# Optimization experiments

Hardware: AMD Instinct MI355X
Metric: run time of the kernel (lower is better)

The kernel has to match this reference:

```python
import jax, jax.numpy as jnp
import numpy as np

NUM_HEADS = 16

def setup_inputs() -> dict:
    key = jax.random.key(0)
    ks = jax.random.split(key, 9)
    B, S, H = 2, 2048, 1024
    sc = 0.02
    return {
        "x":  jax.random.normal(ks[0], (B, S, H), jnp.float32),
        "Wq": jax.random.normal(ks[1], (H, H), jnp.float32) * sc,
        "bq": jnp.zeros((H,), jnp.float32),
        "Wk": jax.random.normal(ks[2], (H, H), jnp.float32) * sc,
        "bk": jnp.zeros((H,), jnp.float32),
        "Wv": jax.random.normal(ks[3], (H, H), jnp.float32) * sc,
        "bv": jnp.zeros((H,), jnp.float32),
        "Wo": jax.random.normal(ks[4], (H, H), jnp.float32) * sc,
        "bo": jnp.zeros((H,), jnp.float32),
    }

def _split_heads(t, nh):
    B, S, H = t.shape
    return t.reshape(B, S, nh, H // nh).transpose(0, 2, 1, 3)  # [B, nh, S, hd]

def reference(x, Wq, bq, Wk, bk, Wv, bv, Wo, bo):
    # mask_type == 'gaussian', dropout = 0 (eval), return_weights = False
    B, S, H = x.shape
    nh = NUM_HEADS
    q = _split_heads(x @ Wq + bq, nh)  # [B, nh, S, hd]
    k = _split_heads(x @ Wk + bk, nh)
    v = _split_heads(x @ Wv + bv, nh)
    dif = q - k  # elementwise, as in the original
    # exp(-dif @ dif^T / 2)
    score = jnp.exp(-0.5 * jnp.einsum('bhqd,bhkd->bhqk', dif, dif))
    # gaussian mask: 1 strictly above the diagonal, 0 on/below (faithful to source)
    mask = jnp.triu(jnp.ones((S, S), x.dtype), k=1)
    prob = score * mask  # [B, nh, S, S]
    ctx = jnp.einsum('bhqk,bhkd->bhqd', prob, v)  # [B, nh, S, hd]
    ctx = ctx.transpose(0, 2, 1, 3).reshape(B, S, H)
    return ctx @ Wo + bo
```

## Files before the change

kernel.cpp:

```cpp
#include <hip/hip_runtime.h>
#include <math.h>

constexpr int SEQ  = 2048;
constexpr int HID  = 1024;
constexpr int MTOT = 4096;
constexpr int BH   = 32;

typedef _Float16 f16;
typedef _Float16 f16x8 __attribute__((ext_vector_type(8)));
typedef float    f32x4 __attribute__((ext_vector_type(4)));

__global__ __launch_bounds__(256) void prep(const float* __restrict__ x,
                                            const float* __restrict__ Wq,
                                            const float* __restrict__ Wk,
                                            const float* __restrict__ Wv,
                                            const float* __restrict__ Wo,
                                            f16* __restrict__ xh,
                                            f16* __restrict__ WqkT,
                                            f16* __restrict__ WvT,
                                            f16* __restrict__ WoT) {
    __shared__ f16 T[64][72];
    const int z = blockIdx.z;
    const int t = threadIdx.x;

    if (z == 3) {
        const int chunk = blockIdx.y * 16 + blockIdx.x;
        const float* src = x + (size_t)chunk * 16384;
        f16* dst = xh + (size_t)chunk * 16384;
#pragma unroll
        for (int it = 0; it < 16; it++) {
            const int i = it * 1024 + t * 4;
            float4 v = *(const float4*)(src + i);
            f16 o[4] = {(f16)v.x, (f16)v.y, (f16)v.z, (f16)v.w};
            *(ushort4*)(dst + i) = *(ushort4*)o;
        }
        return;
    }

    const float* W  = (z == 0) ? Wq : (z == 1) ? Wv : Wo;
    f16* WT = (z == 0) ? WqkT : (z == 1) ? WvT : WoT;
    const int k0 = blockIdx.x * 64, n0 = blockIdx.y * 64;
    const int r  = t >> 4;
    const int c4 = (t & 15) * 4;
#pragma unroll
    for (int rr = 0; rr < 64; rr += 16) {
        float4 w = *(const float4*)(W + (size_t)(k0 + rr + r) * HID + n0 + c4);
        if (z == 0) {
            float4 w2 = *(const float4*)(Wk + (size_t)(k0 + rr + r) * HID + n0 + c4);
            w.x -= w2.x; w.y -= w2.y; w.z -= w2.z; w.w -= w2.w;
        }
        T[c4 + 0][rr + r] = (f16)w.x;
        T[c4 + 1][rr + r] = (f16)w.y;
        T[c4 + 2][rr + r] = (f16)w.z;
        T[c4 + 3][rr + r] = (f16)w.w;
    }
    __syncthreads();
#pragma unroll
    for (int pp = 0; pp < 2; pp++) {
        const int nr = pp * 32 + (t >> 3);
        const int kc = (t & 7) * 8;
        *(uint4*)(WT + (size_t)(n0 + nr) * HID + k0 + kc) = *(uint4*)(&T[nr][kc]);
    }
}

__global__ __launch_bounds__(256, 4) void proj_gemm(const f16* __restrict__ A,
                                                    const f16* __restrict__ WqkT,
                                                    const f16* __restrict__ WvT,
                                                    const float* __restrict__ bq,
                                                    const float* __restrict__ bk,
                                                    const float* __restrict__ bv,
                                                    f16* __restrict__ dif,
                                                    f16* __restrict__ vT) {
    __shared__ f16 As[128 * 72];
    __shared__ f16 Bs[64 * 72];
    const int t = threadIdx.x;
    const int m0  = blockIdx.x * 128;
    const int n0g = blockIdx.y * 64;
    const bool isv = (n0g >= HID);
    const f16* BT = isv ? WvT : WqkT;
    const int n0 = n0g & (HID - 1);
    const int w = t >> 6, l = t & 63, quad = l >> 4, ln = l & 15;
    const int wm = w * 32;
    const int arow = t >> 1, ahalf = (t & 1) * 32;
    const int brow = t >> 2, boff = (t & 3) * 16;

    const f16* pa = A  + (size_t)(m0 + arow) * HID + ahalf;
    const f16* pb = BT + (size_t)(n0 + brow) * HID + boff;

    uint4 ar0 = *(const uint4*)(pa),      ar1 = *(const uint4*)(pa + 8);
    uint4 ar2 = *(const uint4*)(pa + 16), ar3 = *(const uint4*)(pa + 24);
    uint4 br0 = *(const uint4*)(pb),      br1 = *(const uint4*)(pb + 8);

    f32x4 acc[2][4] = {};

    for (int k0 = 0; k0 < HID; k0 += 64) {
        __syncthreads();
        f16* da = As + arow * 72 + ahalf;
        *(uint4*)(da)      = ar0; *(uint4*)(da + 8)  = ar1;
        *(uint4*)(da + 16) = ar2; *(uint4*)(da + 24) = ar3;
        f16* db = Bs + brow * 72 + boff;
        *(uint4*)(db) = br0; *(uint4*)(db + 8) = br1;
        __syncthreads();
        if (k0 + 64 < HID) {
            const f16* qa = pa + k0 + 64;
            const f16* qb = pb + k0 + 64;
            ar0 = *(const uint4*)(qa);      ar1 = *(const uint4*)(qa + 8);
            ar2 = *(const uint4*)(qa + 16); ar3 = *(const uint4*)(qa + 24);
            br0 = *(const uint4*)(qb);      br1 = *(const uint4*)(qb + 8);
        }
#pragma unroll
        for (int kh = 0; kh < 2; kh++) {
            f16x8 af[2], bf[4];
#pragma unroll
            for (int mt = 0; mt < 2; mt++)
                af[mt] = *(const f16x8*)(As + (wm + mt * 16 + ln) * 72 + kh * 32 + quad * 8);
#pragma unroll
            for (int nt = 0; nt < 4; nt++)
                bf[nt] = *(const f16x8*)(Bs + (nt * 16 + ln) * 72 + kh * 32 + quad * 8);
#pragma unroll
            for (int mt = 0; mt < 2; mt++)
#pragma unroll
                for (int nt = 0; nt < 4; nt++)
                    acc[mt][nt] = __builtin_amdgcn_mfma_f32_16x16x32_f16(
                        af[mt], bf[nt], acc[mt][nt], 0, 0, 0);
        }
    }

#pragma unroll
    for (int mt = 0; mt < 2; mt++) {
#pragma unroll
        for (int nt = 0; nt < 4; nt++) {
            const int nl = n0 + nt * 16 + ln;
            const int m_base = m0 + wm + mt * 16 + quad * 4;
            const int h = nl >> 6, e = nl & 63;
            if (!isv) {
                const float bb = bq[nl] - bk[nl];
#pragma unroll
                for (int r = 0; r < 4; r++) {
                    const int m = m_base + r;
                    const int b = m >> 11, s = m & 2047;
                    dif[((size_t)(b * 16 + h) * SEQ + s) * 64 + e] =
                        (f16)(acc[mt][nt][r] + bb);
                }
            } else {
                const float bb = bv[nl];
                const int b = m_base >> 11, s0 = m_base & 2047;
                f16 o[4];
#pragma unroll
                for (int r = 0; r < 4; r++) o[r] = (f16)(acc[mt][nt][r] + bb);
                *(ushort4*)(&vT[((size_t)(b * 16 + h) * 64 + e) * SEQ + s0]) =
                    *(ushort4*)o;
            }
        }
    }
}

__global__ __launch_bounds__(256) void out_gemm(const f16* __restrict__ C0,
                                                const f16* __restrict__ C1,
                                                const f16* __restrict__ WoT,
                                                const float* __restrict__ bo,
                                                float* __restrict__ out) {
    __shared__ f16 As[2][128 * 72];
    __shared__ f16 Bs[2][64 * 72];
    const int t = threadIdx.x;
    const int m0 = blockIdx.x * 128, n0 = blockIdx.y * 64;
    const int w = t >> 6, l = t & 63, quad = l >> 4, ln = l & 15;
    const int wm = (w >> 1) * 64, wn = (w & 1) * 32;
    const int arow = t >> 1, ahalf = (t & 1) * 32;
    const int brow = t >> 2, boff = (t & 3) * 16;

    const f16* pa0 = C0  + (size_t)(m0 + arow) * HID + ahalf;
    const f16* pa1 = C1  + (size_t)(m0 + arow) * HID + ahalf;
    const f16* pb  = WoT + (size_t)(n0 + brow) * HID + boff;

    f16x8 a0 = *(const f16x8*)(pa0)      + *(const f16x8*)(pa1);
    f16x8 a1 = *(const f16x8*)(pa0 + 8)  + *(const f16x8*)(pa1 + 8);
    f16x8 a2 = *(const f16x8*)(pa0 + 16) + *(const f16x8*)(pa1 + 16);
    f16x8 a3 = *(const f16x8*)(pa0 + 24) + *(const f16x8*)(pa1 + 24);
    uint4 b0 = *(const uint4*)(pb), b1 = *(const uint4*)(pb + 8);

    f32x4 acc[4][2] = {};
    int buf = 0;

    for (int k0 = 0; k0 < HID; k0 += 64) {
        f16* da = As[buf] + arow * 72 + ahalf;
        *(f16x8*)(da)      = a0; *(f16x8*)(da + 8)  = a1;
        *(f16x8*)(da + 16) = a2; *(f16x8*)(da + 24) = a3;
        f16* db = Bs[buf] + brow * 72 + boff;
        *(uint4*)(db) = b0; *(uint4*)(db + 8) = b1;
        __syncthreads();
        if (k0 + 64 < HID) {
            const int kn = k0 + 64;
            a0 = *(const f16x8*)(pa0 + kn)      + *(const f16x8*)(pa1 + kn);
            a1 = *(const f16x8*)(pa0 + kn + 8)  + *(const f16x8*)(pa1 + kn + 8);
            a2 = *(const f16x8*)(pa0 + kn + 16) + *(const f16x8*)(pa1 + kn + 16);
            a3 = *(const f16x8*)(pa0 + kn + 24) + *(const f16x8*)(pa1 + kn + 24);
            b0 = *(const uint4*)(pb + kn); b1 = *(const uint4*)(pb + kn + 8);
        }
#pragma unroll
        for (int kh = 0; kh < 2; kh++) {
            f16x8 af[4], bf[2];
#pragma unroll
            for (int mt = 0; mt < 4; mt++)
                af[mt] = *(const f16x8*)(As[buf] + (wm + mt * 16 + ln) * 72 + kh * 32 + quad * 8);
#pragma unroll
            for (int nt = 0; nt < 2; nt++)
                bf[nt] = *(const f16x8*)(Bs[buf] + (wn + nt * 16 + ln) * 72 + kh * 32 + quad * 8);
#pragma unroll
            for (int mt = 0; mt < 4; mt++)
#pragma unroll
                for (int nt = 0; nt < 2; nt++)
                    acc[mt][nt] = __builtin_amdgcn_mfma_f32_16x16x32_f16(
                        af[mt], bf[nt], acc[mt][nt], 0, 0, 0);
        }
        buf ^= 1;
    }

#pragma unroll
    for (int mt = 0; mt < 4; mt++)
#pragma unroll
        for (int nt = 0; nt < 2; nt++) {
            const int n = n0 + wn + nt * 16 + ln;
            const float bb = bo[n];
            const int m_base = m0 + wm + mt * 16 + quad * 4;
#pragma unroll
            for (int r = 0; r < 4; r++)
                out[(size_t)(m_base + r) * HID + n] =
                    acc[mt][nt][r] * 65536.0f + bb;
        }
}

__global__ __launch_bounds__(256) void attn_f16(const f16* __restrict__ dif,
                                                const f16* __restrict__ vT,
                                                f16* __restrict__ ctx0,
                                                f16* __restrict__ ctx1) {
    __shared__ f16 Qs[64 * 72];
    __shared__ f16 Ks[64 * 72];
    __shared__ f16 Vs[64 * 72];
    __shared__ f16 Ps[64 * 72];

    const int pq = blockIdx.x, bh = blockIdx.y, ks = blockIdx.z;
    f16* Cout = ks ? ctx1 : ctx0;
    const f16* D  = dif + (size_t)bh * SEQ * 64;
    const f16* VT = vT  + (size_t)bh * 64 * SEQ;
    const int b = bh >> 4, h = bh & 15;
    const int t = threadIdx.x, w = t >> 6, l = t & 63, quad = l >> 4, ln = l & 15;
    const int ve = t >> 2, vc = (t & 3) * 16;

    for (int half = 0; half < 2; half++) {
        const int qt = half ? (31 - pq) : pq;
        const int i0 = qt * 64;
        __syncthreads();

#pragma unroll
        for (int rr = 0; rr < 2; rr++) {
            const int o = rr * 2048 + t * 8;
            uint4 v = *(const uint4*)(D + i0 * 64 + o);
            *(uint4*)(Qs + (o >> 6) * 72 + (o & 63)) = v;
        }
        __syncthreads();
        f16x8 aq[2];
#pragma unroll
        for (int kh = 0; kh < 2; kh++)
            aq[kh] = *(const f16x8*)(Qs + (w * 16 + ln) * 72 + kh * 32 + quad * 8);

        f32x4 acc[4] = {};
        const int kt0 = qt + ks;

        uint4 kr0, kr1, vr0, vr1;
        if (kt0 < 32) {
            const int j0 = kt0 * 64;
            kr0 = *(const uint4*)(D + j0 * 64 + t * 8);
            kr1 = *(const uint4*)(D + j0 * 64 + 2048 + t * 8);
            vr0 = *(const uint4*)(VT + (size_t)ve * SEQ + j0 + vc);
            vr1 = *(const uint4*)(VT + (size_t)ve * SEQ + j0 + vc + 8);
        }

        for (int kt = kt0; kt < 32; kt += 2) {
            __syncthreads();

            {
                const int o0 = t * 8, o1 = 2048 + t * 8;
                *(uint4*)(Ks + (o0 >> 6) * 72 + (o0 & 63)) = kr0;
                *(uint4*)(Ks + (o1 >> 6) * 72 + (o1 & 63)) = kr1;
                *(uint4*)(Vs + ve * 72 + vc)     = vr0;
                *(uint4*)(Vs + ve * 72 + vc + 8) = vr1;
            }
            __syncthreads();

            if (kt + 2 < 32) {
                const int j2 = (kt + 2) * 64;
                kr0 = *(const uint4*)(D + j2 * 64 + t * 8);
                kr1 = *(const uint4*)(D + j2 * 64 + 2048 + t * 8);
                vr0 = *(const uint4*)(VT + (size_t)ve * SEQ + j2 + vc);
                vr1 = *(const uint4*)(VT + (size_t)ve * SEQ + j2 + vc + 8);
            }

            f32x4 s[4] = {};
#pragma unroll
            for (int kh = 0; kh < 2; kh++)
#pragma unroll
                for (int nt = 0; nt < 4; nt++) {
                    f16x8 bfr = *(const f16x8*)(Ks + (nt * 16 + ln) * 72 + kh * 32 + quad * 8);
                    s[nt] = __builtin_amdgcn_mfma_f32_16x16x32_f16(aq[kh], bfr, s[nt], 0, 0, 0);
                }

            const bool full = (kt > qt);
#pragma unroll
            for (int nt = 0; nt < 4; nt++)
#pragma unroll
                for (int r = 0; r < 4; r++) {
                    const int iloc = w * 16 + quad * 4 + r;
                    const int jloc = nt * 16 + ln;
                    float p = (full || (jloc > iloc))
                                  ? fminf(__expf(fmaf(s[nt][r], -0.5f,
                                                      -11.090354888959125f)), 60000.0f)
                                  : 0.0f;
                    Ps[iloc * 72 + jloc] = (f16)p;
                }

#pragma unroll
            for (int kh = 0; kh < 2; kh++) {
                f16x8 a = *(const f16x8*)(Ps + (w * 16 + ln) * 72 + kh * 32 + quad * 8);
#pragma unroll
                for (int nt = 0; nt < 4; nt++) {
                    f16x8 bfr = *(const f16x8*)(Vs + (nt * 16 + ln) * 72 + kh * 32 + quad * 8);
                    acc[nt] = __builtin_amdgcn_mfma_f32_16x16x32_f16(a, bfr, acc[nt], 0, 0, 0);
                }
            }
        }

#pragma unroll
        for (int nt = 0; nt < 4; nt++)
#pragma unroll
            for (int r = 0; r < 4; r++) {
                const int iloc = w * 16 + quad * 4 + r;
                Cout[(size_t)(b * SEQ + i0 + iloc) * HID + h * 64 + nt * 16 + ln] =
                    (f16)acc[nt][r];
            }
    }
}

extern "C" void kernel_launch(void* const* d_in, const int* in_sizes, int n_in,
                              void* d_out, int out_size, void* d_ws, size_t ws_size,
                              hipStream_t stream) {
    const float* x  = (const float*)d_in[0];
    const float* Wq = (const float*)d_in[1];
    const float* bq = (const float*)d_in[2];
    const float* Wk = (const float*)d_in[3];
    const float* bk = (const float*)d_in[4];
    const float* Wv = (const float*)d_in[5];
    const float* bv = (const float*)d_in[6];
    const float* Wo = (const float*)d_in[7];
    const float* bo = (const float*)d_in[8];
    float* out = (float*)d_out;

    char* ws = (char*)d_ws;
    f16* xh   = (f16*)(ws);
    f16* WqkT = (f16*)(ws + (8 << 20));
    f16* WvT  = (f16*)(ws + (10 << 20));
    f16* WoT  = (f16*)(ws + (12 << 20));
    f16* dif  = (f16*)(ws + (14 << 20));
    f16* vT   = (f16*)(ws + (22 << 20));
    f16* ctx0 = (f16*)(ws + (30 << 20));
    f16* ctx1 = (f16*)(ws + (38 << 20));

    prep<<<dim3(16, 16, 4), 256, 0, stream>>>(x, Wq, Wk, Wv, Wo,
                                              xh, WqkT, WvT, WoT);
    proj_gemm<<<dim3(MTOT / 128, 32), 256, 0, stream>>>(xh, WqkT, WvT,
                                                        bq, bk, bv, dif, vT);
    attn_f16<<<dim3(16, BH, 2), 256, 0, stream>>>(dif, vT, ctx0, ctx1);
    out_gemm<<<dim3(MTOT / 128, 16), 256, 0, stream>>>(ctx0, ctx1, WoT, bo, out);
}
```

Before: 190.8 us.

## Use direct global-to-LDS loads with XOR swizzle and stage projection epilogue through LDS

The projection GEMM now loads A and B tiles with global_load_lds into an XOR-swizzled, unpadded LDS layout instead of going through registers, which should cut register pressure and VGPR-to-LDS store instructions. The epilogue writes results into shared memory first and then emits coalesced 16-byte stores for both the dif and the transposed vT outputs, replacing scattered 2-byte and 8-byte stores. In exchange, the register prefetch of the next k-tile is dropped, so global loads no longer overlap with MFMA work within a block and the loop relies on other resident blocks for latency hiding.

New measurement: 186.7 us. 2.2% less time.

```diff
diff --git a/kernel.cpp b/kernel.cpp
--- a/kernel.cpp
+++ b/kernel.cpp
@@ -9,6 +9,12 @@
 typedef _Float16 f16;
 typedef _Float16 f16x8 __attribute__((ext_vector_type(8)));
 typedef float    f32x4 __attribute__((ext_vector_type(4)));
+
+__device__ __forceinline__ void gld16(const f16* g, f16* l) {
+    __builtin_amdgcn_global_load_lds(
+        (__attribute__((address_space(1))) void*)g,
+        (__attribute__((address_space(3))) void*)l, 16, 0, 0);
+}
 
 __global__ __launch_bounds__(256) void prep(const float* __restrict__ x,
                                             const float* __restrict__ Wq,
@@ -72,7 +78,7 @@
                                                     f16* __restrict__ dif,
                                                     f16* __restrict__ vT) {
     __shared__ f16 As[128 * 72];
-    __shared__ f16 Bs[64 * 72];
+    __shared__ f16 Bs[64 * 64];
     const int t = threadIdx.x;
     const int m0  = blockIdx.x * 128;
     const int n0g = blockIdx.y * 64;
@@ -81,42 +87,40 @@
     const int n0 = n0g & (HID - 1);
     const int w = t >> 6, l = t & 63, quad = l >> 4, ln = l & 15;
     const int wm = w * 32;
-    const int arow = t >> 1, ahalf = (t & 1) * 32;
-    const int brow = t >> 2, boff = (t & 3) * 16;
-
-    const f16* pa = A  + (size_t)(m0 + arow) * HID + ahalf;
-    const f16* pb = BT + (size_t)(n0 + brow) * HID + boff;
-
-    uint4 ar0 = *(const uint4*)(pa),      ar1 = *(const uint4*)(pa + 8);
-    uint4 ar2 = *(const uint4*)(pa + 16), ar3 = *(const uint4*)(pa + 24);
-    uint4 br0 = *(const uint4*)(pb),      br1 = *(const uint4*)(pb + 8);
+    const int xk = ln & 7;
+
+    const int srow8 = l >> 3;
+    const int soct  = (l & 7) ^ srow8;
+    const f16* pa = A  + (size_t)(m0 + w * 32 + srow8) * HID + soct * 8;
+    const f16* pb = BT + (size_t)(n0 + w * 16 + srow8) * HID + soct * 8;
 
     f32x4 acc[2][4] = {};
 
     for (int k0 = 0; k0 < HID; k0 += 64) {
         __syncthreads();
-        f16* da = As + arow * 72 + ahalf;
-        *(uint4*)(da)      = ar0; *(uint4*)(da + 8)  = ar1;
-        *(uint4*)(da + 16) = ar2; *(uint4*)(da + 24) = ar3;
-        f16* db = Bs + brow * 72 + boff;
-        *(uint4*)(db) = br0; *(uint4*)(db + 8) = br1;
-        __syncthreads();
-        if (k0 + 64 < HID) {
-            const f16* qa = pa + k0 + 64;
-            const f16* qb = pb + k0 + 64;
-            ar0 = *(const uint4*)(qa);      ar1 = *(const uint4*)(qa + 8);
-            ar2 = *(const uint4*)(qa + 16); ar3 = *(const uint4*)(qa + 24);
-            br0 = *(const uint4*)(qb);      br1 = *(const uint4*)(qb + 8);
-        }
+#pragma unroll
+        for (int c = 0; c < 4; c++)
+            gld16(pa + (size_t)c * 8 * HID + k0, As + (w * 4 + c) * 512);
+#pragma unroll
+        for (int c = 0; c < 2; c++)
+            gld16(pb + (size_t)c * 8 * HID + k0, Bs + (w * 2 + c) * 512);
+        __syncthreads();
+
 #pragma unroll
         for (int kh = 0; kh < 2; kh++) {
             f16x8 af[2], bf[4];
 #pragma unroll
-            for (int mt = 0; mt < 2; mt++)
-                af[mt] = *(const f16x8*)(As + (wm + mt * 16 + ln) * 72 + kh * 32 + quad * 8);
-#pragma unroll
-            for (int nt = 0; nt < 4; nt++)
-                bf[nt] = *(const f16x8*)(Bs + (nt * 16 + ln) * 72 + kh * 32 + quad * 8);
+            for (int mt = 0; mt < 2; mt++) {
+                const int row = wm + mt * 16 + ln;
+                const int oct = (kh * 4 + quad) ^ xk;
+                af[mt] = *(const f16x8*)(As + row * 64 + oct * 8);
+            }
+#pragma unroll
+            for (int nt = 0; nt < 4; nt++) {
+                const int row = nt * 16 + ln;
+                const int oct = (kh * 4 + quad) ^ xk;
+                bf[nt] = *(const f16x8*)(Bs + row * 64 + oct * 8);
+            }
 #pragma unroll
             for (int mt = 0; mt < 2; mt++)
 #pragma unroll
@@ -126,32 +130,54 @@
         }
     }
 
-#pragma unroll
-    for (int mt = 0; mt < 2; mt++) {
+    __syncthreads();
+    const int b_  = m0 >> 11;
+    const int s0g = m0 & 2047;
+    const int h_  = n0 >> 6;
+
+    if (!isv) {
+        float bb[4];
 #pragma unroll
         for (int nt = 0; nt < 4; nt++) {
             const int nl = n0 + nt * 16 + ln;
-            const int m_base = m0 + wm + mt * 16 + quad * 4;
-            const int h = nl >> 6, e = nl & 63;
-            if (!isv) {
-                const float bb = bq[nl] - bk[nl];
+            bb[nt] = bq[nl] - bk[nl];
+        }
+#pragma unroll
+        for (int mt = 0; mt < 2; mt++)
+#pragma unroll
+            for (int nt = 0; nt < 4; nt++)
 #pragma unroll
                 for (int r = 0; r < 4; r++) {
-                    const int m = m_base + r;
-                    const int b = m >> 11, s = m & 2047;
-                    dif[((size_t)(b * 16 + h) * SEQ + s) * 64 + e] =
-                        (f16)(acc[mt][nt][r] + bb);
+                    const int sl = wm + mt * 16 + quad * 4 + r;
+                    As[sl * 72 + nt * 16 + ln] = (f16)(acc[mt][nt][r] + bb[nt]);
                 }
-            } else {
-                const float bb = bv[nl];
-                const int b = m_base >> 11, s0 = m_base & 2047;
-                f16 o[4];
-#pragma unroll
-                for (int r = 0; r < 4; r++) o[r] = (f16)(acc[mt][nt][r] + bb);
-                *(ushort4*)(&vT[((size_t)(b * 16 + h) * 64 + e) * SEQ + s0]) =
-                    *(ushort4*)o;
-            }
-        }
+        __syncthreads();
+        f16* base = dif + ((size_t)(b_ * 16 + h_) * SEQ + s0g) * 64;
+        const int sl = t >> 1, eo = (t & 1) * 32;
+#pragma unroll
+        for (int i = 0; i < 4; i++)
+            *(uint4*)(base + (size_t)sl * 64 + eo + i * 8) =
+                *(uint4*)(&As[sl * 72 + eo + i * 8]);
+    } else {
+        float bb[4];
+#pragma unroll
+        for (int nt = 0; nt < 4; nt++)
+            bb[nt] = bv[n0 + nt * 16 + ln];
+#pragma unroll
+        for (int mt = 0; mt < 2; mt++)
+#pragma unroll
+            for (int nt = 0; nt < 4; nt++)
+#pragma unroll
+                for (int r = 0; r < 4; r++) {
+                    const int sl = wm + mt * 16 + quad * 4 + r;
+                    As[(nt * 16 + ln) * 136 + sl] = (f16)(acc[mt][nt][r] + bb[nt]);
+                }
+        __syncthreads();
+        const int eb = t >> 2, so = (t & 3) * 32;
+        f16* base = vT + ((size_t)(b_ * 16 + h_) * 64 + eb) * SEQ + s0g + so;
+#pragma unroll
+        for (int i = 0; i < 4; i++)
+            *(uint4*)(base + i * 8) = *(uint4*)(&As[eb * 136 + so + i * 8]);
     }
 }
 
```
